# Optimization experiments

Hardware: AMD Instinct MI355X
Metric: run time of the kernel (lower is better)

## Reference

```python
import jax, jax.numpy as jnp
import numpy as np

T = 4           # timesteps (init kwarg)
GAMA = 1.0      # surrogate-gradient width (unused in pure fwd)
THRESH = 2.0    # initial threshold value
B = 8           # batch size per timestep
FEAT = (1024, 3072)


def setup_inputs() -> dict:
    key = jax.random.key(0)
    x = jax.random.normal(key, (T * B,) + FEAT, dtype=jnp.float32)
    # learned params sized as in __init__
    thresh2 = jnp.full(FEAT, THRESH, dtype=jnp.float32)   # nn.Parameter torch.full((1024,3072), thresh)
    dtmem = jnp.zeros(FEAT, dtype=jnp.float32)            # nn.Parameter ones_like * 0.0
    return {"x": x, "thresh2": thresh2, "dtmem": dtmem}


def reference(x, thresh2, dtmem):
    # non-align, T > 0 branch of IF.forward
    thre = thresh2  # original uses thresh2.data (detached); same values in fwd
    b = x.shape[0] // T
    xs = x.reshape((T, b) + x.shape[1:])            # ExpandTemporalDim: [T, B, 1024, 3072]
    mem0 = jnp.broadcast_to(dtmem * thre, xs.shape[1:])  # initial membrane potential

    def step(mem, x_t):
        mem = mem + x_t
        spike = (mem - thre >= 0).astype(x.dtype) * thre  # ZIF heaviside, scaled by threshold
        mem = mem - spike                                  # soft reset
        return mem, spike

    _, spikes = jax.lax.scan(step, mem0, xs)        # [T, B, 1024, 3072]
    return spikes.reshape((T * b,) + x.shape[1:])   # MergeTemporalDim
```

## Files before the change

kernel.cpp:

```cpp
#include <hip/hip_runtime.h>


constexpr int T_STEPS = 4;
constexpr int B_SZ    = 8;

__global__ __launch_bounds__(256) void if_fwd_kernel(
    const float4* __restrict__ x,
    const float4* __restrict__ thresh2,
    const float4* __restrict__ dtmem,
    float4* __restrict__ out,
    int n4)
{
    const int f = blockIdx.x * blockDim.x + threadIdx.x;
    if (f >= n4) return;

    const float4 th = thresh2[f];
    const float4 dt = dtmem[f];

#pragma unroll
    for (int b = 0; b < B_SZ; ++b) {
        float mx = dt.x * th.x;
        float my = dt.y * th.y;
        float mz = dt.z * th.z;
        float mw = dt.w * th.w;

#pragma unroll
        for (int t = 0; t < T_STEPS; ++t) {
            const long long idx = (long long)(t * B_SZ + b) * n4 + f;
            const float4 xv = x[idx];
            mx += xv.x; my += xv.y; mz += xv.z; mw += xv.w;

            float4 s;
            s.x = (mx - th.x >= 0.0f) ? th.x : 0.0f;
            s.y = (my - th.y >= 0.0f) ? th.y : 0.0f;
            s.z = (mz - th.z >= 0.0f) ? th.z : 0.0f;
            s.w = (mw - th.w >= 0.0f) ? th.w : 0.0f;

            out[idx] = s;

            mx -= s.x; my -= s.y; mz -= s.z; mw -= s.w;
        }
    }
}

extern "C" void kernel_launch(void* const* d_in, const int* in_sizes, int n_in,
                              void* d_out, int out_size, void* d_ws, size_t ws_size,
                              hipStream_t stream) {
    const float* x       = (const float*)d_in[0];
    const float* thresh2 = (const float*)d_in[1];
    const float* dtmem   = (const float*)d_in[2];
    float* out = (float*)d_out;

    const int n  = in_sizes[1];
    const int n4 = n / 4;

    const int block = 256;
    const int grid  = (n4 + block - 1) / block;

    if_fwd_kernel<<<grid, block, 0, stream>>>(
        (const float4*)x, (const float4*)thresh2, (const float4*)dtmem,
        (float4*)out, n4);
}
```

Before: 670.8 us.

## Parallelize over batch in grid and use nontemporal loads/stores

Moves the batch loop into the grid, so each block handles one batch index for a 256-vector feature chunk, giving eight times as many blocks with shorter per-thread chains. Input loads and output stores become nontemporal to avoid polluting cache with streaming data. Thresh and dtmem are now reloaded once per batch index instead of once per thread, which adds a small amount of read traffic.

Result: faster. 641.6 us (-4.4%).

```diff
diff --git a/kernel.cpp b/kernel.cpp
--- a/kernel.cpp
+++ b/kernel.cpp
@@ -1,45 +1,44 @@
 #include <hip/hip_runtime.h>
 
+
+typedef float vf4 __attribute__((ext_vector_type(4)));
 
 constexpr int T_STEPS = 4;
 constexpr int B_SZ    = 8;
 
 __global__ __launch_bounds__(256) void if_fwd_kernel(
-    const float4* __restrict__ x,
-    const float4* __restrict__ thresh2,
-    const float4* __restrict__ dtmem,
-    float4* __restrict__ out,
+    const vf4* __restrict__ x,
+    const vf4* __restrict__ thresh2,
+    const vf4* __restrict__ dtmem,
+    vf4* __restrict__ out,
     int n4)
 {
-    const int f = blockIdx.x * blockDim.x + threadIdx.x;
+    const int bid    = blockIdx.x;
+    const int b      = bid & (B_SZ - 1);
+    const int fchunk = bid >> 3;
+    const int f      = fchunk * 256 + threadIdx.x;
     if (f >= n4) return;
 
-    const float4 th = thresh2[f];
-    const float4 dt = dtmem[f];
+    const vf4 th = thresh2[f];
+    const vf4 dt = dtmem[f];
+
+    vf4 m = dt * th;
 
 #pragma unroll
-    for (int b = 0; b < B_SZ; ++b) {
-        float mx = dt.x * th.x;
-        float my = dt.y * th.y;
-        float mz = dt.z * th.z;
-        float mw = dt.w * th.w;
+    for (int t = 0; t < T_STEPS; ++t) {
+        const long long idx = (long long)(t * B_SZ + b) * n4 + f;
+        const vf4 xv = __builtin_nontemporal_load(&x[idx]);
+        m += xv;
 
-#pragma unroll
-        for (int t = 0; t < T_STEPS; ++t) {
-            const long long idx = (long long)(t * B_SZ + b) * n4 + f;
-            const float4 xv = x[idx];
-            mx += xv.x; my += xv.y; mz += xv.z; mw += xv.w;
+        vf4 s;
+        s.x = (m.x - th.x >= 0.0f) ? th.x : 0.0f;
+        s.y = (m.y - th.y >= 0.0f) ? th.y : 0.0f;
+        s.z = (m.z - th.z >= 0.0f) ? th.z : 0.0f;
+        s.w = (m.w - th.w >= 0.0f) ? th.w : 0.0f;
 
-            float4 s;
-            s.x = (mx - th.x >= 0.0f) ? th.x : 0.0f;
-            s.y = (my - th.y >= 0.0f) ? th.y : 0.0f;
-            s.z = (mz - th.z >= 0.0f) ? th.z : 0.0f;
-            s.w = (mw - th.w >= 0.0f) ? th.w : 0.0f;
+        __builtin_nontemporal_store(s, &out[idx]);
 
-            out[idx] = s;
-
-            mx -= s.x; my -= s.y; mz -= s.z; mw -= s.w;
-        }
+        m -= s;
     }
 }
 
@@ -54,10 +53,11 @@
     const int n  = in_sizes[1];
     const int n4 = n / 4;
 
-    const int block = 256;
-    const int grid  = (n4 + block - 1) / block;
+    const int block   = 256;
+    const int fchunks = (n4 + block - 1) / block;
+    const int grid    = fchunks * B_SZ;
 
     if_fwd_kernel<<<grid, block, 0, stream>>>(
-        (const float4*)x, (const float4*)thresh2, (const float4*)dtmem,
-        (float4*)out, n4);
+        (const vf4*)x, (const vf4*)thresh2, (const vf4*)dtmem,
+        (vf4*)out, n4);
 }
```
